# Performance work log

Hardware: AMD Instinct MI355X
Metric: run time of the kernel (lower is better)

## Reference

```python
import jax, jax.numpy as jnp
from jax import lax
import numpy as np

B, T, F, H = 32, 512, 1024, 1024


def setup_inputs() -> dict:
    key = jax.random.key(0)
    ks = jax.random.split(key, 7)
    s = 0.02
    return {
        "x": jax.random.normal(ks[0], (B, T, F), dtype=jnp.float32),
        "W0": jax.random.normal(ks[1], (F, 4 * H), dtype=jnp.float32) * s,
        "U0": jax.random.normal(ks[2], (H, 4 * H), dtype=jnp.float32) * s,
        "b0": jax.random.normal(ks[3], (4 * H,), dtype=jnp.float32) * s,
        "W1": jax.random.normal(ks[4], (H, 4 * H), dtype=jnp.float32) * s,
        "U1": jax.random.normal(ks[5], (H, 4 * H), dtype=jnp.float32) * s,
        "b1": jax.random.normal(ks[6], (4 * H,), dtype=jnp.float32) * s,
    }


def _lstm(x, W, U, b):
    # x: [B, T, F] -> sequence outputs [B, T, H], final h, final c
    b_, t_, _ = x.shape
    h_dim = U.shape[0]
    # Precompute input projections for all timesteps (batched GEMM).
    xz = jnp.einsum('btf,fg->btg', x, W) + b  # [B, T, 4H]

    def step(carry, xz_t):
        h, c = carry
        z = xz_t + h @ U  # [B, 4H]
        i, f, g, o = jnp.split(z, 4, axis=-1)  # Keras gate order: i, f, c(g), o
        i = jax.nn.sigmoid(i)
        f = jax.nn.sigmoid(f)
        g = jnp.tanh(g)
        o = jax.nn.sigmoid(o)
        c = f * c + i * g
        h = o * jnp.tanh(c)
        return (h, c), h

    h0 = jnp.zeros((b_, h_dim), dtype=x.dtype)
    c0 = jnp.zeros((b_, h_dim), dtype=x.dtype)
    (h, c), hs = lax.scan(step, (h0, c0), jnp.swapaxes(xz, 0, 1))
    return jnp.swapaxes(hs, 0, 1), h, c


def reference(x, W0, U0, b0, W1, U1, b1):
    # Layer 0: return_sequences=True
    seq0, _, _ = _lstm(x, W0, U0, b0)
    # Layer 1: return_state=True -> (last_output, h, c); last_output == h
    _, h1, c1 = _lstm(seq0, W1, U1, b1)
    return (h1, h1, c1)
```

## Files before the change

kernel.cpp:

```cpp
#include <hip/hip_runtime.h>
#include <cstdint>


typedef __attribute__((ext_vector_type(8))) short bf16x8;
typedef __attribute__((ext_vector_type(4))) float f32x4;
typedef __attribute__((ext_vector_type(2))) unsigned int u32x2;

#define XZ0_OFF   0ull
#define XF_OFF    134217728ull
#define W0F_OFF   167772160ull
#define U0F_OFF   176160768ull
#define W1F_OFF   184549376ull
#define WS_TOTAL  201326592ull
#define RING_OFF  XF_OFF
#define H1B_OFF   (XF_OFF + 524288ull)
#define FLG_OFF   (XF_OFF + 655360ull)

__device__ __forceinline__ float bf2f(short s) {
  unsigned int u = ((unsigned int)(unsigned short)s) << 16;
  return __builtin_bit_cast(float, u);
}
__device__ __forceinline__ short f2bf(float f) {
  unsigned int u = __builtin_bit_cast(unsigned int, f);
  u = (u + 0x7fffu + ((u >> 16) & 1u)) >> 16;
  return (short)u;
}
__device__ __forceinline__ void g2l16(const void* g, void* l) {
  __builtin_amdgcn_global_load_lds(
      (const __attribute__((address_space(1))) unsigned int*)g,
      (__attribute__((address_space(3))) unsigned int*)l, 16, 0, 0);
}
__device__ __forceinline__ float sigm(float x) { return 1.f / (1.f + __expf(-x)); }

__device__ __forceinline__ bf16x8 ld16_sc1(const short* p) {
  bf16x8 r;
  asm volatile("global_load_dwordx4 %0, %1, off sc1" : "=&v"(r) : "v"(p));
  return r;
}
__device__ __forceinline__ void st2_sc1(short* p, unsigned v) {
  asm volatile("global_store_short %0, %1, off sc1" :: "v"(p), "v"(v) : "memory");
}
__device__ __forceinline__ void st4_sc1(unsigned* p, unsigned v) {
  asm volatile("global_store_dword %0, %1, off sc1" :: "v"(p), "v"(v) : "memory");
}
#define VM_DRAIN asm volatile("s_waitcnt vmcnt(0)" ::: "memory")

__global__ __launch_bounds__(256) void pack_x(const float* __restrict__ x,
                                              short* __restrict__ dst) {
  int gid = blockIdx.x * 256 + threadIdx.x;
  int lane = gid & 63;
  int unit = gid >> 6;
  int mtile = unit >> 5, kstep = unit & 31;
  int row = mtile * 16 + (lane & 15);
  int k0 = kstep * 32 + ((lane >> 4) << 3);
  const float* s = x + (size_t)row * 1024 + k0;
  bf16x8 v;
#pragma unroll
  for (int j = 0; j < 8; j++) v[j] = f2bf(s[j]);
  *(bf16x8*)(dst + (size_t)gid * 8) = v;
}

__global__ __launch_bounds__(256) void pack_w(const float* __restrict__ src0,
                                              const float* __restrict__ src1,
                                              int ksh, short* __restrict__ dst) {
  int gid = blockIdx.x * 256 + threadIdx.x;
  int lane = gid & 63;
  int unit = gid >> 6;
  int ntile = unit >> ksh;
  int kstep = unit & ((1 << ksh) - 1);
  int col = ntile * 16 + (lane & 15);
  int k0 = kstep * 32 + ((lane >> 4) << 3);
  const float* s = (k0 < 1024) ? src0 : src1;
  int kk = k0 & 1023;
  bf16x8 v;
#pragma unroll
  for (int j = 0; j < 8; j++) v[j] = f2bf(s[(size_t)(kk + j) * 4096 + col]);
  *(bf16x8*)(dst + (size_t)gid * 8) = v;
}

__global__ __launch_bounds__(256) void gemm_xw(const short* __restrict__ xf,
                                               const short* __restrict__ wf,
                                               short* __restrict__ outz) {
  extern __shared__ char smem[];

  int bid = blockIdx.x;
  int swz = (bid & 7) * 512 + (bid >> 3);
  int bn = swz >> 7;
  int bm = swz & 127;

  const int tid = threadIdx.x, wid = tid >> 6, lane = tid & 63;
  const int wm = wid >> 1, wn = wid & 1;
  f32x4 acc[4][4] = {};

  const short* xbase = xf + (size_t)(bm * 8) * 32 * 512;
  const short* wbase = wf + (size_t)(bn * 8) * 32 * 512;

  auto Abuf = [&](int buf) -> short* { return (short*)(smem + buf * 32768); };
  auto Bbuf = [&](int buf) -> short* { return (short*)(smem + 16384 + buf * 32768); };

  auto stage = [&](int buf, int kt) {
    short* A = Abuf(buf);
    short* B = Bbuf(buf);
#pragma unroll
    for (int i = 0; i < 4; i++) {
      int u = wid + 4 * i;
      int mt = u >> 1, ks = u & 1;
      int gk = kt * 2 + ks;
      g2l16(xbase + (size_t)(mt * 32 + gk) * 512 + lane * 8, A + u * 512);
      g2l16(wbase + (size_t)(mt * 32 + gk) * 512 + lane * 8, B + u * 512);
    }
  };

  stage(0, 0);
  __syncthreads();
  for (int kt = 0; kt < 16; kt++) {
    int buf = kt & 1;
    if (kt < 15) stage(buf ^ 1, kt + 1);
    const short* A = Abuf(buf) + (wm * 4) * 1024;
    const short* B = Bbuf(buf) + (wn * 4) * 1024;
#pragma unroll
    for (int ks = 0; ks < 2; ks++) {
      bf16x8 av[4], bv[4];
#pragma unroll
      for (int i = 0; i < 4; i++) av[i] = *(const bf16x8*)(A + (i * 2 + ks) * 512 + lane * 8);
#pragma unroll
      for (int j = 0; j < 4; j++) bv[j] = *(const bf16x8*)(B + (j * 2 + ks) * 512 + lane * 8);
#pragma unroll
      for (int i = 0; i < 4; i++)
#pragma unroll
        for (int j = 0; j < 4; j++)
          acc[i][j] = __builtin_amdgcn_mfma_f32_16x16x32_bf16(av[i], bv[j], acc[i][j], 0, 0, 0);
    }
    __syncthreads();
  }

  int rb = bm * 128 + wm * 64 + ((lane >> 4) << 2);
  int cb = bn * 128 + wn * 64 + (lane & 15);
#pragma unroll
  for (int i = 0; i < 4; i++)
#pragma unroll
    for (int j = 0; j < 4; j++)
#pragma unroll
      for (int r = 0; r < 4; r++) {
        size_t row = rb + i * 16 + r;
        size_t col = cb + j * 16;
        outz[row * 4096 + col] = f2bf(acc[i][j][r]);
      }
}

__global__ __launch_bounds__(256, 1) void lstm_persist(
    const short* __restrict__ xz0, const short* __restrict__ u0f,
    const short* __restrict__ w1u1f, const float* __restrict__ b0,
    const float* __restrict__ b1, short* __restrict__ h0ring,
    short* __restrict__ h1buf, unsigned int* __restrict__ flags,
    float* __restrict__ out) {
  extern __shared__ char smem[];
  short* wlds = (short*)smem;
  float* red = (float*)(smem + 131072);

  const int wg = blockIdx.x;
  const int tid = threadIdx.x;
  const int wid = tid >> 6;
  const int lane = tid & 63;
  const bool l1 = (wg >= 128);
  const int u0 = (wg & 127) * 8;
  const int KS = l1 ? 64 : 32;
  const int ksh = l1 ? 6 : 5;
  const short* wf = l1 ? w1u1f : u0f;

  {
    int c = lane & 15;
    for (int u = wid; u < 2 * KS; u += 4) {
      int tau = u >> ksh;
      int s = u & (KS - 1);
      int gate = tau * 2 + (c >> 3);
      int gc = gate * 1024 + u0 + (c & 7);
      int lanep = (lane & 48) + (gc & 15);
      const short* src = wf + ((size_t)(((gc >> 4) << ksh) + s) * 64 + lanep) * 8;
      g2l16(src, wlds + (tau * KS + s) * 512);
    }
  }
  __syncthreads();

  const int bl = (tid & 127) >> 3;
  const int uu = tid & 7;
  const int lrow = bl >> 2, reg = bl & 3;
  float bias[4];
  {
    const float* bb = l1 ? b1 : b0;
#pragma unroll
    for (int g = 0; g < 4; g++) bias[g] = bb[g * 1024 + u0 + uu];
  }

  unsigned int* ownbase = flags + (l1 ? 256 : 0);
  unsigned int* othbase = flags + (l1 ? 0 : 256);

  auto waitfor = [&](int g, unsigned own_t, unsigned oth_t) {
    if ((own_t | oth_t) != 0 && wid == 0) {
      const unsigned* po = ownbase + g * 128 + lane * 2;
      const unsigned* pe = othbase + g * 128 + lane * 2;
      for (int it = 0; it < (1 << 22); ++it) {
        u32x2 ov, ev;
        asm volatile(
            "global_load_dwordx2 %0, %2, off sc1\n\t"
            "global_load_dwordx2 %1, %3, off sc1\n\t"
            "s_waitcnt vmcnt(0)"
            : "=&v"(ov), "=&v"(ev)
            : "v"(po), "v"(pe)
            : "memory");
        if (__all(ov[0] >= own_t && ov[1] >= own_t &&
                  ev[0] >= oth_t && ev[1] >= oth_t)) break;
        asm volatile("s_sleep 1");
      }
    }
    __syncthreads();
  };

  auto gates = [&](const float* xzv, float& cst, short* hw, bool dump, int g) {
    float z[4];
#pragma unroll
    for (int g4 = 0; g4 < 4; g4++) {
      int tau = g4 >> 1;
      int lp = lrow * 16 + (g4 & 1) * 8 + uu;
      float s = bias[g4] + xzv[g4];
#pragma unroll
      for (int w4 = 0; w4 < 4; w4++)
        s += red[((w4 * 2 + tau) * 64 + lp) * 4 + reg];
      z[g4] = s;
    }
    float gi = sigm(z[0]);
    float gf = sigm(z[1]);
    float gg = tanhf(z[2]);
    float go = sigm(z[3]);
    cst = gf * cst + gi * gg;
    float hv = go * tanhf(cst);
    st2_sc1(hw + (g * 16 + bl) * 1024 + u0 + uu,
            (unsigned)(unsigned short)f2bf(hv));
    if (dump) {
      int oi = (g * 16 + bl) * 1024 + u0 + uu;
      out[oi] = hv;
      out[32768 + oi] = hv;
      out[65536 + oi] = cst;
    }
  };

  auto release = [&](int g, unsigned v) {
    VM_DRAIN;
    __syncthreads();
    if (tid == 0) st4_sc1(ownbase + g * 128 + (wg & 127), v);
  };

  if (!l1) {
    auto mini0 = [&](const int g, const int t, float& cst) {
      unsigned short xr0 = 0, xr1 = 0, xr2 = 0, xr3 = 0;
      if (tid < 128) {
        const unsigned short* xp = (const unsigned short*)xz0 +
            (size_t)((g * 16 + bl) * 512 + t) * 4096 + u0 + uu;
        xr0 = xp[0]; xr1 = xp[1024]; xr2 = xp[2048]; xr3 = xp[3072];
      }
      waitfor(g, (unsigned)t, (t >= 8) ? (unsigned)(t - 7) : 0u);
      const short* ap = h0ring + (size_t)((t - 1) & 7) * 32768 +
                        (g * 16 + (lane & 15)) * 1024 + (wid << 8) +
                        ((lane >> 4) << 3);
      bf16x8 a[8];
#pragma unroll
      for (int ks = 0; ks < 8; ks++) a[ks] = ld16_sc1(ap + ks * 32);
      VM_DRAIN;
      __builtin_amdgcn_sched_barrier(0);
      f32x4 acc[2] = {};
#pragma unroll
      for (int ks = 0; ks < 8; ks++) {
        bf16x8 bt0 = *(const bf16x8*)(wlds + (wid * 8 + ks) * 512 + lane * 8);
        bf16x8 bt1 = *(const bf16x8*)(wlds + (32 + wid * 8 + ks) * 512 + lane * 8);
        acc[0] = __builtin_amdgcn_mfma_f32_16x16x32_bf16(a[ks], bt0, acc[0], 0, 0, 0);
        acc[1] = __builtin_amdgcn_mfma_f32_16x16x32_bf16(a[ks], bt1, acc[1], 0, 0, 0);
      }
#pragma unroll
      for (int tau = 0; tau < 2; tau++)
        *(f32x4*)(red + ((wid * 2 + tau) * 64 + lane) * 4) = acc[tau];
      __syncthreads();
      if (tid < 128) {
        float xzv[4] = {bf2f((short)xr0), bf2f((short)xr1),
                        bf2f((short)xr2), bf2f((short)xr3)};
        gates(xzv, cst, h0ring + (size_t)(t & 7) * 32768, false, g);
      }
      release(g, (unsigned)(t + 1));
    };
    float c0 = 0.f, c1 = 0.f;
    for (int t = 0; t < 512; ++t) { mini0(0, t, c0); mini0(1, t, c1); }
  } else {
    auto mini1 = [&](const int g, const int t, float& cst) {
      waitfor(g, (unsigned)t, (unsigned)(t + 1));
      const short* Ab = (wid < 2) ? (h0ring + (size_t)(t & 7) * 32768)
                                  : (h1buf + (size_t)((t - 1) & 1) * 32768);
      const short* ap = Ab + (g * 16 + (lane & 15)) * 1024 + ((wid & 1) << 9) +
                        ((lane >> 4) << 3);
      bf16x8 a[2][8];
#pragma unroll
      for (int half = 0; half < 2; half++)
#pragma unroll
        for (int ks = 0; ks < 8; ks++)
          a[half][ks] = ld16_sc1(ap + half * 256 + ks * 32);
      VM_DRAIN;
      __builtin_amdgcn_sched_barrier(0);
      f32x4 acc[2] = {};
#pragma unroll
      for (int half = 0; half < 2; half++) {
        const int rb = wid * 16 + half * 8;
#pragma unroll
        for (int ks = 0; ks < 8; ks++) {
          bf16x8 bt0 = *(const bf16x8*)(wlds + (rb + ks) * 512 + lane * 8);
          bf16x8 bt1 = *(const bf16x8*)(wlds + (64 + rb + ks) * 512 + lane * 8);
          acc[0] = __builtin_amdgcn_mfma_f32_16x16x32_bf16(a[half][ks], bt0, acc[0], 0, 0, 0);
          acc[1] = __builtin_amdgcn_mfma_f32_16x16x32_bf16(a[half][ks], bt1, acc[1], 0, 0, 0);
        }
      }
#pragma unroll
      for (int tau = 0; tau < 2; tau++)
        *(f32x4*)(red + ((wid * 2 + tau) * 64 + lane) * 4) = acc[tau];
      __syncthreads();
      if (tid < 128) {
        float xzv[4] = {0.f, 0.f, 0.f, 0.f};
        gates(xzv, cst, h1buf + (size_t)(t & 1) * 32768, t == 511, g);
      }
      release(g, (unsigned)(t + 1));
    };
    float c0 = 0.f, c1 = 0.f;
    for (int t = 0; t < 512; ++t) { mini1(0, t, c0); mini1(1, t, c1); }
  }
}

extern "C" void kernel_launch(void* const* d_in, const int* in_sizes, int n_in,
                              void* d_out, int out_size, void* d_ws, size_t ws_size,
                              hipStream_t stream) {
  const float* x  = (const float*)d_in[0];
  const float* W0 = (const float*)d_in[1];
  const float* U0 = (const float*)d_in[2];
  const float* b0 = (const float*)d_in[3];
  const float* W1 = (const float*)d_in[4];
  const float* U1 = (const float*)d_in[5];
  const float* b1 = (const float*)d_in[6];
  char* ws = (char*)d_ws;
  if (ws_size < WS_TOTAL) return;

  short* xz0p = (short*)(ws + XZ0_OFF);
  short* xfp  = (short*)(ws + XF_OFF);
  short* w0fp = (short*)(ws + W0F_OFF);
  short* u0fp = (short*)(ws + U0F_OFF);
  short* w1fp = (short*)(ws + W1F_OFF);
  short* ringp = (short*)(ws + RING_OFF);
  short* h1p   = (short*)(ws + H1B_OFF);
  unsigned int* flagp = (unsigned int*)(ws + FLG_OFF);
  float* outp = (float*)d_out;

  (void)hipFuncSetAttribute((const void*)gemm_xw,
      hipFuncAttributeMaxDynamicSharedMemorySize, 65536);
  (void)hipFuncSetAttribute((const void*)lstm_persist,
      hipFuncAttributeMaxDynamicSharedMemorySize, 147456);

  hipLaunchKernelGGL(pack_x, dim3(8192), dim3(256), 0, stream, x, xfp);
  hipLaunchKernelGGL(pack_w, dim3(2048), dim3(256), 0, stream, W0, W0, 5, w0fp);
  hipLaunchKernelGGL(pack_w, dim3(2048), dim3(256), 0, stream, U0, U0, 5, u0fp);
  hipLaunchKernelGGL(pack_w, dim3(4096), dim3(256), 0, stream, W1, U1, 6, w1fp);
  hipLaunchKernelGGL(gemm_xw, dim3(4096), dim3(256), 65536, stream, xfp, w0fp, xz0p);

  (void)hipMemsetAsync(ws + RING_OFF, 0, 524288 + 131072 + 4096, stream);

  const short* xz0c = xz0p;
  const short* u0fc = u0fp;
  const short* w1fc = w1fp;
  void* kargs[9] = {(void*)&xz0c, (void*)&u0fc, (void*)&w1fc,
                    (void*)&b0,   (void*)&b1,
                    (void*)&ringp, (void*)&h1p, (void*)&flagp, (void*)&outp};
  (void)hipLaunchCooperativeKernel((const void*)lstm_persist, dim3(256), dim3(256),
                                   kargs, 147456u, stream);
}
```

Before: 4.051 ms.

## Merge both batch-group mini-steps into one synchronised step per timestep

The persistent LSTM kernel used to run two separate mini-steps per timestep, one per 16-row batch group, each with its own flag poll, barrier and release. Now each timestep polls the flags for both groups at once with wider loads and issues the h loads for both groups together. It computes the two groups' MFMAs into separate reduction buffers, with a partial vmcnt wait so the second group's loads overlap the first group's MFMAs, and releases both flags together. This halves the number of cross-workgroup synchronisation rounds, at the cost of more registers and losing the pipelining between groups that split steps allowed.

```diff
diff --git a/kernel.cpp b/kernel.cpp
--- a/kernel.cpp
+++ b/kernel.cpp
@@ -4,7 +4,7 @@
 
 typedef __attribute__((ext_vector_type(8))) short bf16x8;
 typedef __attribute__((ext_vector_type(4))) float f32x4;
-typedef __attribute__((ext_vector_type(2))) unsigned int u32x2;
+typedef __attribute__((ext_vector_type(4))) unsigned int u32x4;
 
 #define XZ0_OFF   0ull
 #define XF_OFF    134217728ull
@@ -44,6 +44,9 @@
   asm volatile("global_store_dword %0, %1, off sc1" :: "v"(p), "v"(v) : "memory");
 }
 #define VM_DRAIN asm volatile("s_waitcnt vmcnt(0)" ::: "memory")
+#define VM_WAIT8 asm volatile("s_waitcnt vmcnt(8)" ::: "memory")
+#define VM_WAIT16 asm volatile("s_waitcnt vmcnt(16)" ::: "memory")
+#define SBAR __builtin_amdgcn_sched_barrier(0)
 
 __global__ __launch_bounds__(256) void pack_x(const float* __restrict__ x,
                                               short* __restrict__ dst) {
@@ -156,7 +159,8 @@
     float* __restrict__ out) {
   extern __shared__ char smem[];
   short* wlds = (short*)smem;
-  float* red = (float*)(smem + 131072);
+  float* red0 = (float*)(smem + 131072);
+  float* red1 = (float*)(smem + 139264);
 
   const int wg = blockIdx.x;
   const int tid = threadIdx.x;
@@ -195,37 +199,40 @@
   unsigned int* ownbase = flags + (l1 ? 256 : 0);
   unsigned int* othbase = flags + (l1 ? 0 : 256);
 
-  auto waitfor = [&](int g, unsigned own_t, unsigned oth_t) {
+  auto pollboth = [&](unsigned own_t, unsigned oth_t) {
     if ((own_t | oth_t) != 0 && wid == 0) {
-      const unsigned* po = ownbase + g * 128 + lane * 2;
-      const unsigned* pe = othbase + g * 128 + lane * 2;
+      const unsigned* po = ownbase + lane * 4;
+      const unsigned* pe = othbase + lane * 4;
       for (int it = 0; it < (1 << 22); ++it) {
-        u32x2 ov, ev;
+        u32x4 ov, ev;
         asm volatile(
-            "global_load_dwordx2 %0, %2, off sc1\n\t"
-            "global_load_dwordx2 %1, %3, off sc1\n\t"
+            "global_load_dwordx4 %0, %2, off sc1\n\t"
+            "global_load_dwordx4 %1, %3, off sc1\n\t"
             "s_waitcnt vmcnt(0)"
             : "=&v"(ov), "=&v"(ev)
             : "v"(po), "v"(pe)
             : "memory");
         if (__all(ov[0] >= own_t && ov[1] >= own_t &&
-                  ev[0] >= oth_t && ev[1] >= oth_t)) break;
+                  ov[2] >= own_t && ov[3] >= own_t &&
+                  ev[0] >= oth_t && ev[1] >= oth_t &&
+                  ev[2] >= oth_t && ev[3] >= oth_t)) break;
         asm volatile("s_sleep 1");
       }
     }
     __syncthreads();
   };
 
-  auto gates = [&](const float* xzv, float& cst, short* hw, bool dump, int g) {
-    float z[4];
+  auto gates1 = [&](const float* rd, float xz0v, float xz1v, float xz2v, float xz3v,
+                    float& cst, short* hw, bool dump, int g) {
+    float z[4] = {xz0v, xz1v, xz2v, xz3v};
 #pragma unroll
     for (int g4 = 0; g4 < 4; g4++) {
       int tau = g4 >> 1;
       int lp = lrow * 16 + (g4 & 1) * 8 + uu;
-      float s = bias[g4] + xzv[g4];
+      float s = bias[g4] + z[g4];
 #pragma unroll
       for (int w4 = 0; w4 < 4; w4++)
-        s += red[((w4 * 2 + tau) * 64 + lp) * 4 + reg];
+        s += rd[((w4 * 2 + tau) * 64 + lp) * 4 + reg];
       z[g4] = s;
     }
     float gi = sigm(z[0]);
@@ -244,66 +251,100 @@
     }
   };
 
-  auto release = [&](int g, unsigned v) {
-    VM_DRAIN;
-    __syncthreads();
-    if (tid == 0) st4_sc1(ownbase + g * 128 + (wg & 127), v);
-  };
-
   if (!l1) {
-    auto mini0 = [&](const int g, const int t, float& cst) {
-      unsigned short xr0 = 0, xr1 = 0, xr2 = 0, xr3 = 0;
+    const int kb = wid << 8;
+    float c0 = 0.f, c1 = 0.f;
+    for (int t = 0; t < 512; ++t) {
+      unsigned short xr[2][4];
       if (tid < 128) {
-        const unsigned short* xp = (const unsigned short*)xz0 +
-            (size_t)((g * 16 + bl) * 512 + t) * 4096 + u0 + uu;
-        xr0 = xp[0]; xr1 = xp[1024]; xr2 = xp[2048]; xr3 = xp[3072];
-      }
-      waitfor(g, (unsigned)t, (t >= 8) ? (unsigned)(t - 7) : 0u);
-      const short* ap = h0ring + (size_t)((t - 1) & 7) * 32768 +
-                        (g * 16 + (lane & 15)) * 1024 + (wid << 8) +
-                        ((lane >> 4) << 3);
-      bf16x8 a[8];
-#pragma unroll
-      for (int ks = 0; ks < 8; ks++) a[ks] = ld16_sc1(ap + ks * 32);
-      VM_DRAIN;
-      __builtin_amdgcn_sched_barrier(0);
-      f32x4 acc[2] = {};
+#pragma unroll
+        for (int g = 0; g < 2; g++) {
+          const unsigned short* xp = (const unsigned short*)xz0 +
+              (size_t)((g * 16 + bl) * 512 + t) * 4096 + u0 + uu;
+          xr[g][0] = xp[0]; xr[g][1] = xp[1024];
+          xr[g][2] = xp[2048]; xr[g][3] = xp[3072];
+        }
+      } else {
+        xr[0][0] = xr[0][1] = xr[0][2] = xr[0][3] = 0;
+        xr[1][0] = xr[1][1] = xr[1][2] = xr[1][3] = 0;
+      }
+      SBAR;
+      pollboth((unsigned)t, (t >= 8) ? (unsigned)(t - 7) : 0u);
+      SBAR;
+      const short* base = h0ring + (size_t)((t - 1) & 7) * 32768 +
+                          (lane & 15) * 1024 + kb + ((lane >> 4) << 3);
+      bf16x8 a0[8], a1[8];
+#pragma unroll
+      for (int ks = 0; ks < 8; ks++) a0[ks] = ld16_sc1(base + ks * 32);
+#pragma unroll
+      for (int ks = 0; ks < 8; ks++) a1[ks] = ld16_sc1(base + 16384 + ks * 32);
+      SBAR;
+      VM_WAIT8;
+      SBAR;
+      f32x4 acc0[2] = {};
 #pragma unroll
       for (int ks = 0; ks < 8; ks++) {
         bf16x8 bt0 = *(const bf16x8*)(wlds + (wid * 8 + ks) * 512 + lane * 8);
         bf16x8 bt1 = *(const bf16x8*)(wlds + (32 + wid * 8 + ks) * 512 + lane * 8);
-        acc[0] = __builtin_amdgcn_mfma_f32_16x16x32_bf16(a[ks], bt0, acc[0], 0, 0, 0);
-        acc[1] = __builtin_amdgcn_mfma_f32_16x16x32_bf16(a[ks], bt1, acc[1], 0, 0, 0);
+        acc0[0] = __builtin_amdgcn_mfma_f32_16x16x32_bf16(a0[ks], bt0, acc0[0], 0, 0, 0);
+        acc0[1] = __builtin_amdgcn_mfma_f32_16x16x32_bf16(a0[ks], bt1, acc0[1], 0, 0, 0);
       }
 #pragma unroll
       for (int tau = 0; tau < 2; tau++)
-        *(f32x4*)(red + ((wid * 2 + tau) * 64 + lane) * 4) = acc[tau];
+        *(f32x4*)(red0 + ((wid * 2 + tau) * 64 + lane) * 4) = acc0[tau];
+      SBAR;
+      VM_DRAIN;
+      SBAR;
+      f32x4 acc1[2] = {};
+#pragma unroll
+      for (int ks = 0; ks < 8; ks++) {
+        bf16x8 bt0 = *(const bf16x8*)(wlds + (wid * 8 + ks) * 512 + lane * 8);
+        bf16x8 bt1 = *(const bf16x8*)(wlds + (32 + wid * 8 + ks) * 512 + lane * 8);
+        acc1[0] = __builtin_amdgcn_mfma_f32_16x16x32_bf16(a1[ks], bt0, acc1[0], 0, 0, 0);
+        acc1[1] = __builtin_amdgcn_mfma_f32_16x16x32_bf16(a1[ks], bt1, acc1[1], 0, 0, 0);
+      }
+#pragma unroll
+      for (int tau = 0; tau < 2; tau++)
+        *(f32x4*)(red1 + ((wid * 2 + tau) * 64 + lane) * 4) = acc1[tau];
       __syncthreads();
       if (tid < 128) {
-        float xzv[4] = {bf2f((short)xr0), bf2f((short)xr1),
-                        bf2f((short)xr2), bf2f((short)xr3)};
-        gates(xzv, cst, h0ring + (size_t)(t & 7) * 32768, false, g);
-      }
-      release(g, (unsigned)(t + 1));
-    };
+        short* hw = h0ring + (size_t)(t & 7) * 32768;
+        gates1(red0, bf2f((short)xr[0][0]), bf2f((short)xr[0][1]),
+               bf2f((short)xr[0][2]), bf2f((short)xr[0][3]), c0, hw, false, 0);
+        gates1(red1, bf2f((short)xr[1][0]), bf2f((short)xr[1][1]),
+               bf2f((short)xr[1][2]), bf2f((short)xr[1][3]), c1, hw, false, 1);
+      }
+      VM_DRAIN;
+      __syncthreads();
+      if (tid == 0) {
+        st4_sc1(ownbase + (wg & 127), (unsigned)(t + 1));
+        st4_sc1(ownbase + 128 + (wg & 127), (unsigned)(t + 1));
+      }
+    }
+  } else {
     float c0 = 0.f, c1 = 0.f;
-    for (int t = 0; t < 512; ++t) { mini0(0, t, c0); mini0(1, t, c1); }
-  } else {
-    auto mini1 = [&](const int g, const int t, float& cst) {
-      waitfor(g, (unsigned)t, (unsigned)(t + 1));
+    for (int t = 0; t < 512; ++t) {
+      pollboth((unsigned)t, (unsigned)(t + 1));
+      SBAR;
       const short* Ab = (wid < 2) ? (h0ring + (size_t)(t & 7) * 32768)
                                   : (h1buf + (size_t)((t - 1) & 1) * 32768);
-      const short* ap = Ab + (g * 16 + (lane & 15)) * 1024 + ((wid & 1) << 9) +
-                        ((lane >> 4) << 3);
-      bf16x8 a[2][8];
+      const short* base = Ab + (lane & 15) * 1024 + ((wid & 1) << 9) +
+                          ((lane >> 4) << 3);
+      bf16x8 a0[2][8], a1[2][8];
 #pragma unroll
       for (int half = 0; half < 2; half++)
 #pragma unroll
         for (int ks = 0; ks < 8; ks++)
-          a[half][ks] = ld16_sc1(ap + half * 256 + ks * 32);
-      VM_DRAIN;
-      __builtin_amdgcn_sched_barrier(0);
-      f32x4 acc[2] = {};
+          a0[half][ks] = ld16_sc1(base + half * 256 + ks * 32);
+#pragma unroll
+      for (int half = 0; half < 2; half++)
+#pragma unroll
+        for (int ks = 0; ks < 8; ks++)
+          a1[half][ks] = ld16_sc1(base + 16384 + half * 256 + ks * 32);
+      SBAR;
+      VM_WAIT16;
+      SBAR;
+      f32x4 acc0[2] = {};
 #pragma unroll
       for (int half = 0; half < 2; half++) {
         const int rb = wid * 16 + half * 8;
@@ -311,22 +352,44 @@
         for (int ks = 0; ks < 8; ks++) {
           bf16x8 bt0 = *(const bf16x8*)(wlds + (rb + ks) * 512 + lane * 8);
           bf16x8 bt1 = *(const bf16x8*)(wlds + (64 + rb + ks) * 512 + lane * 8);
-          acc[0] = __builtin_amdgcn_mfma_f32_16x16x32_bf16(a[half][ks], bt0, acc[0], 0, 0, 0);
-          acc[1] = __builtin_amdgcn_mfma_f32_16x16x32_bf16(a[half][ks], bt1, acc[1], 0, 0, 0);
+          acc0[0] = __builtin_amdgcn_mfma_f32_16x16x32_bf16(a0[half][ks], bt0, acc0[0], 0, 0, 0);
+          acc0[1] = __builtin_amdgcn_mfma_f32_16x16x32_bf16(a0[half][ks], bt1, acc0[1], 0, 0, 0);
         }
       }
 #pragma unroll
       for (int tau = 0; tau < 2; tau++)
-        *(f32x4*)(red + ((wid * 2 + tau) * 64 + lane) * 4) = acc[tau];
+        *(f32x4*)(red0 + ((wid * 2 + tau) * 64 + lane) * 4) = acc0[tau];
+      SBAR;
+      VM_DRAIN;
+      SBAR;
+      f32x4 acc1[2] = {};
+#pragma unroll
+      for (int half = 0; half < 2; half++) {
+        const int rb = wid * 16 + half * 8;
+#pragma unroll
+        for (int ks = 0; ks < 8; ks++) {
+          bf16x8 bt0 = *(const bf16x8*)(wlds + (rb + ks) * 512 + lane * 8);
+          bf16x8 bt1 = *(const bf16x8*)(wlds + (64 + rb + ks) * 512 + lane * 8);
+          acc1[0] = __builtin_amdgcn_mfma_f32_16x16x32_bf16(a1[half][ks], bt0, acc1[0], 0, 0, 0);
+          acc1[1] = __builtin_amdgcn_mfma_f32_16x16x32_bf16(a1[half][ks], bt1, acc1[1], 0, 0, 0);
+        }
+      }
+#pragma unroll
+      for (int tau = 0; tau < 2; tau++)
+        *(f32x4*)(red1 + ((wid * 2 + tau) * 64 + lane) * 4) = acc1[tau];
       __syncthreads();
       if (tid < 128) {
-        float xzv[4] = {0.f, 0.f, 0.f, 0.f};
-        gates(xzv, cst, h1buf + (size_t)(t & 1) * 32768, t == 511, g);
-      }
-      release(g, (unsigned)(t + 1));
-    };
-    float c0 = 0.f, c1 = 0.f;
-    for (int t = 0; t < 512; ++t) { mini1(0, t, c0); mini1(1, t, c1); }
+        short* hw = h1buf + (size_t)(t & 1) * 32768;
+        gates1(red0, 0.f, 0.f, 0.f, 0.f, c0, hw, t == 511, 0);
+        gates1(red1, 0.f, 0.f, 0.f, 0.f, c1, hw, t == 511, 1);
+      }
+      VM_DRAIN;
+      __syncthreads();
+      if (tid == 0) {
+        st4_sc1(ownbase + (wg & 127), (unsigned)(t + 1));
+        st4_sc1(ownbase + 128 + (wg & 127), (unsigned)(t + 1));
+      }
+    }
   }
 }
 
```

Result: slower. 5.008 ms (+23.6%).

## Overlap flag polling with gate math and interleave xz gates per unit

Applied to the files above, without the earlier changes.

Moves the spin-wait for the other batch group's dependencies off the critical path: idle waves 2 and 3 poll the next mini-step's flags while waves 0-1 compute the gate nonlinearities, which removes one barrier-bounded wait per step. The reduction buffer is double-buffered per group so the two groups do not collide. The xz0 GEMM output is re-laid out so the four gate values for a unit sit next to each other and can be fetched with one 8-byte load issued alongside the h loads. The cost is more intricate cross-wave synchronisation that depends on barriers to order polling correctly.

```diff
diff --git a/kernel.cpp b/kernel.cpp
--- a/kernel.cpp
+++ b/kernel.cpp
@@ -3,6 +3,7 @@
 
 
 typedef __attribute__((ext_vector_type(8))) short bf16x8;
+typedef __attribute__((ext_vector_type(4))) short s16x4;
 typedef __attribute__((ext_vector_type(4))) float f32x4;
 typedef __attribute__((ext_vector_type(2))) unsigned int u32x2;
 
@@ -44,6 +45,7 @@
   asm volatile("global_store_dword %0, %1, off sc1" :: "v"(p), "v"(v) : "memory");
 }
 #define VM_DRAIN asm volatile("s_waitcnt vmcnt(0)" ::: "memory")
+#define SBAR __builtin_amdgcn_sched_barrier(0)
 
 __global__ __launch_bounds__(256) void pack_x(const float* __restrict__ x,
                                               short* __restrict__ dst) {
@@ -143,8 +145,8 @@
 #pragma unroll
       for (int r = 0; r < 4; r++) {
         size_t row = rb + i * 16 + r;
-        size_t col = cb + j * 16;
-        outz[row * 4096 + col] = f2bf(acc[i][j][r]);
+        int col = cb + j * 16;
+        outz[row * 4096 + (size_t)(col & 1023) * 4 + (col >> 10)] = f2bf(acc[i][j][r]);
       }
 }
 
@@ -156,7 +158,8 @@
     float* __restrict__ out) {
   extern __shared__ char smem[];
   short* wlds = (short*)smem;
-  float* red = (float*)(smem + 131072);
+  float* red0 = (float*)(smem + 131072);
+  float* red1 = (float*)(smem + 139264);
 
   const int wg = blockIdx.x;
   const int tid = threadIdx.x;
@@ -195,37 +198,36 @@
   unsigned int* ownbase = flags + (l1 ? 256 : 0);
   unsigned int* othbase = flags + (l1 ? 0 : 256);
 
-  auto waitfor = [&](int g, unsigned own_t, unsigned oth_t) {
-    if ((own_t | oth_t) != 0 && wid == 0) {
-      const unsigned* po = ownbase + g * 128 + lane * 2;
-      const unsigned* pe = othbase + g * 128 + lane * 2;
-      for (int it = 0; it < (1 << 22); ++it) {
-        u32x2 ov, ev;
-        asm volatile(
-            "global_load_dwordx2 %0, %2, off sc1\n\t"
-            "global_load_dwordx2 %1, %3, off sc1\n\t"
-            "s_waitcnt vmcnt(0)"
-            : "=&v"(ov), "=&v"(ev)
-            : "v"(po), "v"(pe)
-            : "memory");
-        if (__all(ov[0] >= own_t && ov[1] >= own_t &&
-                  ev[0] >= oth_t && ev[1] >= oth_t)) break;
-        asm volatile("s_sleep 1");
-      }
-    }
-    __syncthreads();
+  auto pollq = [&](int q, unsigned own_t, unsigned oth_t) {
+    if ((own_t | oth_t) == 0) return;
+    const unsigned* po = ownbase + q * 128 + lane * 2;
+    const unsigned* pe = othbase + q * 128 + lane * 2;
+    for (int it = 0; it < (1 << 22); ++it) {
+      u32x2 ov, ev;
+      asm volatile(
+          "global_load_dwordx2 %0, %2, off sc1\n\t"
+          "global_load_dwordx2 %1, %3, off sc1\n\t"
+          "s_waitcnt vmcnt(0)"
+          : "=&v"(ov), "=&v"(ev)
+          : "v"(po), "v"(pe)
+          : "memory");
+      if (__all(ov[0] >= own_t && ov[1] >= own_t &&
+                ev[0] >= oth_t && ev[1] >= oth_t)) break;
+      asm volatile("s_sleep 1");
+    }
   };
 
-  auto gates = [&](const float* xzv, float& cst, short* hw, bool dump, int g) {
+  auto gates1 = [&](const float* rd, s16x4 xv, float& cst, short* hw,
+                    bool dump, int g) {
     float z[4];
 #pragma unroll
     for (int g4 = 0; g4 < 4; g4++) {
       int tau = g4 >> 1;
       int lp = lrow * 16 + (g4 & 1) * 8 + uu;
-      float s = bias[g4] + xzv[g4];
+      float s = bias[g4] + bf2f(xv[g4]);
 #pragma unroll
       for (int w4 = 0; w4 < 4; w4++)
-        s += red[((w4 * 2 + tau) * 64 + lp) * 4 + reg];
+        s += rd[((w4 * 2 + tau) * 64 + lp) * 4 + reg];
       z[g4] = s;
     }
     float gi = sigm(z[0]);
@@ -244,29 +246,20 @@
     }
   };
 
-  auto release = [&](int g, unsigned v) {
-    VM_DRAIN;
-    __syncthreads();
-    if (tid == 0) st4_sc1(ownbase + g * 128 + (wg & 127), v);
-  };
-
   if (!l1) {
-    auto mini0 = [&](const int g, const int t, float& cst) {
-      unsigned short xr0 = 0, xr1 = 0, xr2 = 0, xr3 = 0;
-      if (tid < 128) {
-        const unsigned short* xp = (const unsigned short*)xz0 +
-            (size_t)((g * 16 + bl) * 512 + t) * 4096 + u0 + uu;
-        xr0 = xp[0]; xr1 = xp[1024]; xr2 = xp[2048]; xr3 = xp[3072];
-      }
-      waitfor(g, (unsigned)t, (t >= 8) ? (unsigned)(t - 7) : 0u);
+    float c0 = 0.f, c1 = 0.f;
+    auto mini = [&](int g, int t, float& cst) {
       const short* ap = h0ring + (size_t)((t - 1) & 7) * 32768 +
                         (g * 16 + (lane & 15)) * 1024 + (wid << 8) +
                         ((lane >> 4) << 3);
       bf16x8 a[8];
 #pragma unroll
       for (int ks = 0; ks < 8; ks++) a[ks] = ld16_sc1(ap + ks * 32);
-      VM_DRAIN;
-      __builtin_amdgcn_sched_barrier(0);
+      s16x4 xv = {0, 0, 0, 0};
+      if (tid < 128)
+        xv = *(const s16x4*)(xz0 +
+              ((size_t)((g * 16 + bl) * 512 + t) * 1024 + u0 + uu) * 4);
+      SBAR; VM_DRAIN; SBAR;
       f32x4 acc[2] = {};
 #pragma unroll
       for (int ks = 0; ks < 8; ks++) {
@@ -275,22 +268,28 @@
         acc[0] = __builtin_amdgcn_mfma_f32_16x16x32_bf16(a[ks], bt0, acc[0], 0, 0, 0);
         acc[1] = __builtin_amdgcn_mfma_f32_16x16x32_bf16(a[ks], bt1, acc[1], 0, 0, 0);
       }
+      float* rd = g ? red1 : red0;
 #pragma unroll
       for (int tau = 0; tau < 2; tau++)
-        *(f32x4*)(red + ((wid * 2 + tau) * 64 + lane) * 4) = acc[tau];
+        *(f32x4*)(rd + ((wid * 2 + tau) * 64 + lane) * 4) = acc[tau];
       __syncthreads();
       if (tid < 128) {
-        float xzv[4] = {bf2f((short)xr0), bf2f((short)xr1),
-                        bf2f((short)xr2), bf2f((short)xr3)};
-        gates(xzv, cst, h0ring + (size_t)(t & 7) * 32768, false, g);
-      }
-      release(g, (unsigned)(t + 1));
+        gates1(rd, xv, cst, h0ring + (size_t)(t & 7) * 32768, false, g);
+      } else if (wid == 2 && g == 0) {
+        pollq(1, (unsigned)t, (t >= 8) ? (unsigned)(t - 7) : 0u);
+      } else if (wid == 3 && g == 1 && t < 511) {
+        pollq(0, (unsigned)(t + 1), (t + 1 >= 8) ? (unsigned)(t - 6) : 0u);
+      }
+      VM_DRAIN;
+      __syncthreads();
+      if (tid == 0) st4_sc1(ownbase + g * 128 + (wg & 127), (unsigned)(t + 1));
     };
+    for (int t = 0; t < 512; ++t) { mini(0, t, c0); mini(1, t, c1); }
+  } else {
     float c0 = 0.f, c1 = 0.f;
-    for (int t = 0; t < 512; ++t) { mini0(0, t, c0); mini0(1, t, c1); }
-  } else {
-    auto mini1 = [&](const int g, const int t, float& cst) {
-      waitfor(g, (unsigned)t, (unsigned)(t + 1));
+    if (wid == 3) pollq(0, 0u, 1u);
+    __syncthreads();
+    auto mini = [&](int g, int t, float& cst) {
       const short* Ab = (wid < 2) ? (h0ring + (size_t)(t & 7) * 32768)
                                   : (h1buf + (size_t)((t - 1) & 1) * 32768);
       const short* ap = Ab + (g * 16 + (lane & 15)) * 1024 + ((wid & 1) << 9) +
@@ -301,8 +300,7 @@
 #pragma unroll
         for (int ks = 0; ks < 8; ks++)
           a[half][ks] = ld16_sc1(ap + half * 256 + ks * 32);
-      VM_DRAIN;
-      __builtin_amdgcn_sched_barrier(0);
+      SBAR; VM_DRAIN; SBAR;
       f32x4 acc[2] = {};
 #pragma unroll
       for (int half = 0; half < 2; half++) {
@@ -315,18 +313,24 @@
           acc[1] = __builtin_amdgcn_mfma_f32_16x16x32_bf16(a[half][ks], bt1, acc[1], 0, 0, 0);
         }
       }
+      float* rd = g ? red1 : red0;
 #pragma unroll
       for (int tau = 0; tau < 2; tau++)
-        *(f32x4*)(red + ((wid * 2 + tau) * 64 + lane) * 4) = acc[tau];
+        *(f32x4*)(rd + ((wid * 2 + tau) * 64 + lane) * 4) = acc[tau];
       __syncthreads();
       if (tid < 128) {
-        float xzv[4] = {0.f, 0.f, 0.f, 0.f};
-        gates(xzv, cst, h1buf + (size_t)(t & 1) * 32768, t == 511, g);
-      }
-      release(g, (unsigned)(t + 1));
+        s16x4 zv = {0, 0, 0, 0};
+        gates1(rd, zv, cst, h1buf + (size_t)(t & 1) * 32768, t == 511, g);
+      } else if (wid == 2 && g == 0) {
+        pollq(1, (unsigned)t, (unsigned)(t + 1));
+      } else if (wid == 3 && g == 1 && t < 511) {
+        pollq(0, (unsigned)(t + 1), (unsigned)(t + 2));
+      }
+      VM_DRAIN;
+      __syncthreads();
+      if (tid == 0) st4_sc1(ownbase + g * 128 + (wg & 127), (unsigned)(t + 1));
     };
-    float c0 = 0.f, c1 = 0.f;
-    for (int t = 0; t < 512; ++t) { mini1(0, t, c0); mini1(1, t, c1); }
+    for (int t = 0; t < 512; ++t) { mini(0, t, c0); mini(1, t, c1); }
   }
 }
 
```

Measured after the change: 3.919 ms (median of 2 runs). 3.2% less time.
